# Kernel optimization log

Hardware: AMD Instinct MI355X
Metric: run time of the kernel (lower is better)

The kernel has to match this reference:

```python
import jax, jax.numpy as jnp
import numpy as np

FP8_MAX = 448.0  # float8_e4m3fn max representable magnitude


def _to_fp8(x):
    # round-to-nearest fp8_e4m3 simulation via dtype cast
    return jnp.clip(x, -FP8_MAX, FP8_MAX).astype(jnp.float8_e4m3fn).astype(jnp.float32)


def setup_inputs() -> dict:
    key = jax.random.key(0)
    ks = jax.random.split(key, 8)
    T, H, I, E, K = 4096, 2048, 4096, 8, 2

    x = jax.random.normal(ks[0], (T, H), dtype=jnp.float32)
    selected_experts = jax.random.randint(ks[1], (T, K), 0, E, dtype=jnp.int32)
    rw = jax.random.uniform(ks[2], (T, K), dtype=jnp.float32) + 1e-3
    routing_weights = rw / jnp.sum(rw, axis=-1, keepdims=True)

    # float master weights -> per-tensor fp8 quantized buffers + weight scales
    w1_f = jax.random.normal(ks[3], (E, 2 * I, H), dtype=jnp.float32) * 0.02
    w2_f = jax.random.normal(ks[4], (E, H, I), dtype=jnp.float32) * 0.02
    w1_wscale = jnp.max(jnp.abs(w1_f), axis=(1, 2)) / FP8_MAX  # [E]
    w2_wscale = jnp.max(jnp.abs(w2_f), axis=(1, 2)) / FP8_MAX
    w1 = _to_fp8(w1_f / w1_wscale[:, None, None])  # fp8 values stored as f32
    w2 = _to_fp8(w2_f / w2_wscale[:, None, None])

    # per-tensor activation input scales (amax-style calibration constants)
    w1_iscale = jnp.full((E,), 4.0 / FP8_MAX, dtype=jnp.float32)
    w2_iscale = jnp.full((E,), 8.0 / FP8_MAX, dtype=jnp.float32)

    return {
        "x": x,
        "selected_experts": selected_experts,
        "routing_weights": routing_weights,
        "w1": w1,
        "w2": w2,
        "w1_iscale": w1_iscale,
        "w2_iscale": w2_iscale,
        "w1_wscale": w1_wscale,
        "w2_wscale": w2_wscale,
    }


def _fp8_linear(x, w_fp8, iscale, wscale):
    xq = _to_fp8(x / iscale)  # [T, in]
    return (xq @ w_fp8.T) * (iscale * wscale)  # [T, out]


def reference(x, selected_experts, routing_weights, w1, w2,
              w1_iscale, w2_iscale, w1_wscale, w2_wscale):
    E = w1.shape[0]
    I = w2.shape[2]
    out = jnp.zeros_like(x)
    for e in range(E):  # fixed small expert loop
        # combined routing weight for this expert per token: [T]
        gate = jnp.sum(
            jnp.where(selected_experts == e, routing_weights, 0.0), axis=-1)
        h = _fp8_linear(x, w1[e], w1_iscale[e], w1_wscale[e])  # [T, 2I]
        g, u = h[:, :I], h[:, I:]
        a = jax.nn.silu(g) * u  # gated activation
        y = _fp8_linear(a, w2[e], w2_iscale[e], w2_wscale[e])  # [T, H]
        out = out + gate[:, None] * y
    return out
```

## Files before the change

kernel.cpp:

```cpp
#include <hip/hip_runtime.h>
#include <cstdint>
#include <cstddef>

#define T_TOK 4096
#define H_DIM 2048
#define I_DIM 4096
#define E_NUM 8
#define CAP_ROWS 9216

#define OFF_COUNTS   0
#define OFF_CURSOR   64
#define OFF_PADOFF   128
#define OFF_TOKIDX   1024
#define OFF_TOKGATE  (OFF_TOKIDX + CAP_ROWS*4)
#define OFF_XQ       ((size_t)(OFF_TOKGATE + CAP_ROWS*4))
#define XQ_BYTES     ((size_t)CAP_ROWS*H_DIM*2)
#define OFF_AQ       (OFF_XQ + XQ_BYTES)
#define AQ_BYTES     ((size_t)CAP_ROWS*I_DIM*2)
#define OFF_W1B      (OFF_AQ + AQ_BYTES)
#define W1B_BYTES    ((size_t)E_NUM*2*I_DIM*H_DIM*2)
#define OFF_W2B      (OFF_W1B + W1B_BYTES)

typedef __bf16 bf16x8 __attribute__((ext_vector_type(8)));
typedef float  f32x4  __attribute__((ext_vector_type(4)));

__device__ __forceinline__ unsigned short bf16hi(float f) {
  return (unsigned short)(__float_as_uint(f) >> 16);
}

__device__ __forceinline__ float fp8_round(float v) {
  v = fminf(448.f, fmaxf(-448.f, v));
  float av = fabsf(v);
  if (av < 0.015625f) {
    return rintf(v * 512.f) * (1.f / 512.f);
  }
  unsigned u = __float_as_uint(v);
  unsigned lsb = (u >> 20) & 1u;
  u += 0x7FFFFu + lsb;
  u &= 0xFFF00000u;
  return __uint_as_float(u);
}

__device__ __forceinline__ void gld16(const void* g, void* l) {
  __builtin_amdgcn_global_load_lds(
      (__attribute__((address_space(1))) void*)((void*)g),
      (__attribute__((address_space(3))) void*)l, 16, 0, 0);
}

__global__ void k_count(const int* __restrict__ se, int* __restrict__ counts) {
  int t = blockIdx.x * 256 + threadIdx.x;
  if (t >= T_TOK) return;
  int e0 = se[t * 2], e1 = se[t * 2 + 1];
  atomicAdd(&counts[e0], 1);
  if (e1 != e0) atomicAdd(&counts[e1], 1);
}

__global__ void k_offsets(const int* __restrict__ counts, int* __restrict__ padOff) {
  if (threadIdx.x == 0 && blockIdx.x == 0) {
    int acc = 0;
    for (int e = 0; e < E_NUM; e++) {
      padOff[e] = acc;
      acc += ((counts[e] + 127) / 128) * 128;
    }
    padOff[E_NUM] = acc;
  }
}

__global__ void k_fill(const int* __restrict__ se, const float* __restrict__ rw,
                       const int* __restrict__ padOff, int* __restrict__ cursor,
                       int* __restrict__ tokIdx, float* __restrict__ tokGate) {
  int t = blockIdx.x * 256 + threadIdx.x;
  if (t >= T_TOK) return;
  int e0 = se[t * 2], e1 = se[t * 2 + 1];
  float w0 = rw[t * 2], w1 = rw[t * 2 + 1];
  float g0 = w0 + (e1 == e0 ? w1 : 0.f);
  int s0 = atomicAdd(&cursor[e0], 1);
  tokIdx[padOff[e0] + s0] = t;
  tokGate[padOff[e0] + s0] = g0;
  if (e1 != e0) {
    int s1 = atomicAdd(&cursor[e1], 1);
    tokIdx[padOff[e1] + s1] = t;
    tokGate[padOff[e1] + s1] = w1;
  }
}

__global__ __launch_bounds__(256)
void k_gather(const float* __restrict__ x, const int* __restrict__ padOff,
              const int* __restrict__ counts, const int* __restrict__ tokIdx,
              const float* __restrict__ w1_is, unsigned short* __restrict__ xq) {
  const int rblk = blockIdx.x;
  const int total = padOff[E_NUM];
  if (rblk >= total) return;
  int e = 0;
  while (rblk >= padOff[e + 1]) e++;
  unsigned short* dst = xq + (size_t)rblk * H_DIM;
  const int c = threadIdx.x * 8;
  const int local = rblk - padOff[e];
  if (local >= counts[e]) {
    uint4 z = {0u, 0u, 0u, 0u};
    *(uint4*)(dst + c) = z;
    return;
  }
  const int tok = tokIdx[rblk];
  const float is = w1_is[e];
  const float* src = x + (size_t)tok * H_DIM + c;
  float4 v0 = *(const float4*)(src);
  float4 v1 = *(const float4*)(src + 4);
  float q0 = fp8_round(v0.x / is), q1 = fp8_round(v0.y / is);
  float q2 = fp8_round(v0.z / is), q3 = fp8_round(v0.w / is);
  float q4 = fp8_round(v1.x / is), q5 = fp8_round(v1.y / is);
  float q6 = fp8_round(v1.z / is), q7 = fp8_round(v1.w / is);
  uint4 o;
  o.x = (unsigned)bf16hi(q0) | ((unsigned)bf16hi(q1) << 16);
  o.y = (unsigned)bf16hi(q2) | ((unsigned)bf16hi(q3) << 16);
  o.z = (unsigned)bf16hi(q4) | ((unsigned)bf16hi(q5) << 16);
  o.w = (unsigned)bf16hi(q6) | ((unsigned)bf16hi(q7) << 16);
  *(uint4*)(dst + c) = o;
}

__global__ __launch_bounds__(256)
void k_wconv(const float* __restrict__ w, unsigned short* __restrict__ o, long n4) {
  long i = (long)blockIdx.x * 256 + threadIdx.x;
  if (i >= n4) return;
  float4 v = ((const float4*)w)[i];
  ushort4 r;
  r.x = bf16hi(v.x); r.y = bf16hi(v.y); r.z = bf16hi(v.z); r.w = bf16hi(v.w);
  ((ushort4*)o)[i] = r;
}

__global__ __launch_bounds__(512, 1)
void k_gemm1(const unsigned short* __restrict__ xq,
             const unsigned short* __restrict__ w1b,
             const int* __restrict__ padOff,
             const float* __restrict__ w1_is, const float* __restrict__ w1_ws,
             const float* __restrict__ w2_is,
             unsigned short* __restrict__ aq) {
  const int e = blockIdx.z;
  const int rbase = padOff[e];
  const int rows = padOff[e + 1] - rbase;
  const int mt = blockIdx.y;
  if (mt * 128 >= rows) return;
  const int nt = blockIdx.x;

  __shared__ __align__(16) unsigned short As[128 * 32];
  __shared__ __align__(16) unsigned short Bg[128 * 32];
  __shared__ __align__(16) unsigned short Bu[128 * 32];

  const int tid = threadIdx.x;
  const int lane = tid & 63;
  const int wave = tid >> 6;
  const int wm = wave >> 2, wn = wave & 3;
  const int lr = lane & 15, quad = lane >> 4;

  const int r = tid >> 2;
  const int kb = tid & 3;
  const unsigned short* pa = xq + (size_t)(rbase + mt * 128 + r) * H_DIM + kb * 8;
  const unsigned short* pg = w1b + ((size_t)e * 2 * I_DIM + nt * 128 + r) * H_DIM + kb * 8;
  const unsigned short* pu = pg + (size_t)I_DIM * H_DIM;
  unsigned short* la = As + tid * 8;
  unsigned short* lg = Bg + tid * 8;
  unsigned short* lu = Bu + tid * 8;

  f32x4 accg[4][2] = {};
  f32x4 accu[4][2] = {};

  for (int k0 = 0; k0 < H_DIM; k0 += 32) {
    gld16(pa + k0, la);
    gld16(pg + k0, lg);
    gld16(pu + k0, lu);
    __syncthreads();
    bf16x8 af[4], gf[2], uf[2];
#pragma unroll
    for (int i = 0; i < 4; i++)
      af[i] = *(const bf16x8*)(As + (wm * 64 + i * 16 + lr) * 32 + quad * 8);
#pragma unroll
    for (int j = 0; j < 2; j++) {
      gf[j] = *(const bf16x8*)(Bg + (wn * 32 + j * 16 + lr) * 32 + quad * 8);
      uf[j] = *(const bf16x8*)(Bu + (wn * 32 + j * 16 + lr) * 32 + quad * 8);
    }
#pragma unroll
    for (int i = 0; i < 4; i++)
#pragma unroll
      for (int j = 0; j < 2; j++) {
        accg[i][j] = __builtin_amdgcn_mfma_f32_16x16x32_bf16(af[i], gf[j], accg[i][j], 0, 0, 0);
        accu[i][j] = __builtin_amdgcn_mfma_f32_16x16x32_bf16(af[i], uf[j], accu[i][j], 0, 0, 0);
      }
    __syncthreads();
  }

  const float s1 = w1_is[e] * w1_ws[e];
  const float is2 = w2_is[e];
#pragma unroll
  for (int i = 0; i < 4; i++)
#pragma unroll
    for (int j = 0; j < 2; j++)
#pragma unroll
      for (int rr = 0; rr < 4; rr++) {
        const int row = wm * 64 + i * 16 + quad * 4 + rr;
        const int col = nt * 128 + wn * 32 + j * 16 + lr;
        float g = accg[i][j][rr] * s1;
        float u = accu[i][j][rr] * s1;
        float a = (g / (1.f + expf(-g))) * u;
        float q = fp8_round(a / is2);
        aq[(size_t)(rbase + mt * 128 + row) * I_DIM + col] = bf16hi(q);
      }
}

__global__ __launch_bounds__(512, 1)
void k_gemm2(const unsigned short* __restrict__ aq,
             const unsigned short* __restrict__ w2b,
             const int* __restrict__ padOff, const int* __restrict__ counts,
             const int* __restrict__ tokIdx, const float* __restrict__ tokGate,
             const float* __restrict__ w2_is, const float* __restrict__ w2_ws,
             float* __restrict__ out) {
  const int e = blockIdx.z;
  const int rbase = padOff[e];
  const int rows = padOff[e + 1] - rbase;
  const int mt = blockIdx.y;
  if (mt * 128 >= rows) return;
  const int nt = blockIdx.x;
  const int cnt = counts[e];

  __shared__ __align__(16) unsigned short As[128 * 32];
  __shared__ __align__(16) unsigned short Bs[128 * 32];
  __shared__ int sTok[128];
  __shared__ float sGate[128];

  const int tid = threadIdx.x;
  const int lane = tid & 63;
  const int wave = tid >> 6;
  const int wm = wave >> 2, wn = wave & 3;
  const int lr = lane & 15, quad = lane >> 4;

  if (tid < 128) {
    int rr = mt * 128 + tid;
    if (rr < cnt) { sTok[tid] = tokIdx[rbase + rr]; sGate[tid] = tokGate[rbase + rr]; }
    else          { sTok[tid] = -1;                 sGate[tid] = 0.f; }
  }

  const int r = tid >> 2;
  const int kb = tid & 3;
  const unsigned short* pa = aq + (size_t)(rbase + mt * 128 + r) * I_DIM + kb * 8;
  const unsigned short* pb = w2b + ((size_t)e * H_DIM + nt * 128 + r) * I_DIM + kb * 8;
  unsigned short* la = As + tid * 8;
  unsigned short* lb = Bs + tid * 8;

  f32x4 acc[4][2] = {};

  for (int k0 = 0; k0 < I_DIM; k0 += 32) {
    gld16(pa + k0, la);
    gld16(pb + k0, lb);
    __syncthreads();
    bf16x8 af[4], bf[2];
#pragma unroll
    for (int i = 0; i < 4; i++)
      af[i] = *(const bf16x8*)(As + (wm * 64 + i * 16 + lr) * 32 + quad * 8);
#pragma unroll
    for (int j = 0; j < 2; j++)
      bf[j] = *(const bf16x8*)(Bs + (wn * 32 + j * 16 + lr) * 32 + quad * 8);
#pragma unroll
    for (int i = 0; i < 4; i++)
#pragma unroll
      for (int j = 0; j < 2; j++)
        acc[i][j] = __builtin_amdgcn_mfma_f32_16x16x32_bf16(af[i], bf[j], acc[i][j], 0, 0, 0);
    __syncthreads();
  }

  const float s2 = w2_is[e] * w2_ws[e];
#pragma unroll
  for (int i = 0; i < 4; i++)
#pragma unroll
    for (int j = 0; j < 2; j++)
#pragma unroll
      for (int rr = 0; rr < 4; rr++) {
        const int row = wm * 64 + i * 16 + quad * 4 + rr;
        const int tk = sTok[row];
        if (tk >= 0) {
          const int col = nt * 128 + wn * 32 + j * 16 + lr;
          unsafeAtomicAdd(out + (size_t)tk * H_DIM + col, sGate[row] * s2 * acc[i][j][rr]);
        }
      }
}

extern "C" void kernel_launch(void* const* d_in, const int* in_sizes, int n_in,
                              void* d_out, int out_size, void* d_ws, size_t ws_size,
                              hipStream_t stream) {
  const float* x     = (const float*)d_in[0];
  const int*   se    = (const int*)d_in[1];
  const float* rw    = (const float*)d_in[2];
  const float* w1    = (const float*)d_in[3];
  const float* w2    = (const float*)d_in[4];
  const float* w1_is = (const float*)d_in[5];
  const float* w2_is = (const float*)d_in[6];
  const float* w1_ws = (const float*)d_in[7];
  const float* w2_ws = (const float*)d_in[8];
  float* out = (float*)d_out;
  char* ws = (char*)d_ws;

  int*   counts  = (int*)(ws + OFF_COUNTS);
  int*   cursor  = (int*)(ws + OFF_CURSOR);
  int*   padOff  = (int*)(ws + OFF_PADOFF);
  int*   tokIdx  = (int*)(ws + OFF_TOKIDX);
  float* tokGate = (float*)(ws + OFF_TOKGATE);
  unsigned short* xq  = (unsigned short*)(ws + OFF_XQ);
  unsigned short* aq  = (unsigned short*)(ws + OFF_AQ);
  unsigned short* w1b = (unsigned short*)(ws + OFF_W1B);
  unsigned short* w2b = (unsigned short*)(ws + OFF_W2B);

  hipMemsetAsync(ws, 0, 1024, stream);
  hipMemsetAsync(d_out, 0, (size_t)T_TOK * H_DIM * sizeof(float), stream);

  k_count  <<<16, 256, 0, stream>>>(se, counts);
  k_offsets<<<1, 1, 0, stream>>>(counts, padOff);
  k_fill   <<<16, 256, 0, stream>>>(se, rw, padOff, cursor, tokIdx, tokGate);
  k_gather <<<CAP_ROWS, 256, 0, stream>>>(x, padOff, counts, tokIdx, w1_is, xq);

  k_wconv<<<131072, 256, 0, stream>>>(w1, w1b, (long)E_NUM * 2 * I_DIM * H_DIM / 4);
  k_wconv<<< 65536, 256, 0, stream>>>(w2, w2b, (long)E_NUM * H_DIM * I_DIM / 4);

  dim3 g1(I_DIM / 128, 32, E_NUM);
  k_gemm1<<<g1, 512, 0, stream>>>(xq, w1b, padOff, w1_is, w1_ws, w2_is, aq);

  dim3 g2(H_DIM / 128, 32, E_NUM);
  k_gemm2<<<g2, 512, 0, stream>>>(aq, w2b, padOff, counts, tokIdx, tokGate, w2_is, w2_ws, out);
}
```

Measured before the change: 1.590 ms.

## Switch expert GEMMs from bf16 to native fp8 MFMA with swizzled LDS

Stores quantized activations and weights as packed e4m3 bytes instead of bf16, and runs both expert GEMMs with the fp8 MFMA instruction over a 64-wide K tile. This halves the bytes moved for weights and activations, including the weight conversion writes, and uses the higher-throughput fp8 matrix path. It also adds an XOR swizzle on the LDS layout to reduce bank conflicts. Correctness now depends on the hand-written fp8 encoder matching e4m3fn for subnormals and on the byte-ordering assumptions of the fp8 MFMA operands.

```diff
diff --git a/kernel.cpp b/kernel.cpp
--- a/kernel.cpp
+++ b/kernel.cpp
@@ -14,19 +14,14 @@
 #define OFF_TOKIDX   1024
 #define OFF_TOKGATE  (OFF_TOKIDX + CAP_ROWS*4)
 #define OFF_XQ       ((size_t)(OFF_TOKGATE + CAP_ROWS*4))
-#define XQ_BYTES     ((size_t)CAP_ROWS*H_DIM*2)
+#define XQ_BYTES     ((size_t)CAP_ROWS*H_DIM)
 #define OFF_AQ       (OFF_XQ + XQ_BYTES)
-#define AQ_BYTES     ((size_t)CAP_ROWS*I_DIM*2)
+#define AQ_BYTES     ((size_t)CAP_ROWS*I_DIM)
 #define OFF_W1B      (OFF_AQ + AQ_BYTES)
-#define W1B_BYTES    ((size_t)E_NUM*2*I_DIM*H_DIM*2)
+#define W1B_BYTES    ((size_t)E_NUM*2*I_DIM*H_DIM)
 #define OFF_W2B      (OFF_W1B + W1B_BYTES)
 
-typedef __bf16 bf16x8 __attribute__((ext_vector_type(8)));
-typedef float  f32x4  __attribute__((ext_vector_type(4)));
-
-__device__ __forceinline__ unsigned short bf16hi(float f) {
-  return (unsigned short)(__float_as_uint(f) >> 16);
-}
+typedef float f32x4 __attribute__((ext_vector_type(4)));
 
 __device__ __forceinline__ float fp8_round(float v) {
   v = fminf(448.f, fmaxf(-448.f, v));
@@ -39,6 +34,18 @@
   u += 0x7FFFFu + lsb;
   u &= 0xFFF00000u;
   return __uint_as_float(u);
+}
+
+__device__ __forceinline__ unsigned fp8_enc(float q) {
+  unsigned u = __float_as_uint(q);
+  unsigned s = (u >> 24) & 0x80u;
+  float aq = fabsf(q);
+  if (aq < 0.015625f) {
+    return s | (unsigned)(int)rintf(aq * 512.f);
+  }
+  unsigned e = (u >> 23) & 0xFFu;
+  unsigned man = (u >> 20) & 7u;
+  return s | ((e - 120u) << 3) | man;
 }
 
 __device__ __forceinline__ void gld16(const void* g, void* l) {
@@ -87,18 +94,17 @@
 __global__ __launch_bounds__(256)
 void k_gather(const float* __restrict__ x, const int* __restrict__ padOff,
               const int* __restrict__ counts, const int* __restrict__ tokIdx,
-              const float* __restrict__ w1_is, unsigned short* __restrict__ xq) {
+              const float* __restrict__ w1_is, unsigned char* __restrict__ xq) {
   const int rblk = blockIdx.x;
   const int total = padOff[E_NUM];
   if (rblk >= total) return;
   int e = 0;
   while (rblk >= padOff[e + 1]) e++;
-  unsigned short* dst = xq + (size_t)rblk * H_DIM;
+  unsigned char* dst = xq + (size_t)rblk * H_DIM;
   const int c = threadIdx.x * 8;
   const int local = rblk - padOff[e];
   if (local >= counts[e]) {
-    uint4 z = {0u, 0u, 0u, 0u};
-    *(uint4*)(dst + c) = z;
+    *(uint2*)(dst + c) = make_uint2(0u, 0u);
     return;
   }
   const int tok = tokIdx[rblk];
@@ -106,35 +112,36 @@
   const float* src = x + (size_t)tok * H_DIM + c;
   float4 v0 = *(const float4*)(src);
   float4 v1 = *(const float4*)(src + 4);
-  float q0 = fp8_round(v0.x / is), q1 = fp8_round(v0.y / is);
-  float q2 = fp8_round(v0.z / is), q3 = fp8_round(v0.w / is);
-  float q4 = fp8_round(v1.x / is), q5 = fp8_round(v1.y / is);
-  float q6 = fp8_round(v1.z / is), q7 = fp8_round(v1.w / is);
-  uint4 o;
-  o.x = (unsigned)bf16hi(q0) | ((unsigned)bf16hi(q1) << 16);
-  o.y = (unsigned)bf16hi(q2) | ((unsigned)bf16hi(q3) << 16);
-  o.z = (unsigned)bf16hi(q4) | ((unsigned)bf16hi(q5) << 16);
-  o.w = (unsigned)bf16hi(q6) | ((unsigned)bf16hi(q7) << 16);
-  *(uint4*)(dst + c) = o;
+  unsigned lo = fp8_enc(fp8_round(v0.x / is))
+              | (fp8_enc(fp8_round(v0.y / is)) << 8)
+              | (fp8_enc(fp8_round(v0.z / is)) << 16)
+              | (fp8_enc(fp8_round(v0.w / is)) << 24);
+  unsigned hi = fp8_enc(fp8_round(v1.x / is))
+              | (fp8_enc(fp8_round(v1.y / is)) << 8)
+              | (fp8_enc(fp8_round(v1.z / is)) << 16)
+              | (fp8_enc(fp8_round(v1.w / is)) << 24);
+  *(uint2*)(dst + c) = make_uint2(lo, hi);
 }
 
 __global__ __launch_bounds__(256)
-void k_wconv(const float* __restrict__ w, unsigned short* __restrict__ o, long n4) {
+void k_wconv(const float* __restrict__ w, unsigned char* __restrict__ o, long n8) {
   long i = (long)blockIdx.x * 256 + threadIdx.x;
-  if (i >= n4) return;
-  float4 v = ((const float4*)w)[i];
-  ushort4 r;
-  r.x = bf16hi(v.x); r.y = bf16hi(v.y); r.z = bf16hi(v.z); r.w = bf16hi(v.w);
-  ((ushort4*)o)[i] = r;
+  if (i >= n8) return;
+  const float4* src = (const float4*)w + i * 2;
+  float4 v0 = src[0];
+  float4 v1 = src[1];
+  unsigned lo = fp8_enc(v0.x) | (fp8_enc(v0.y) << 8) | (fp8_enc(v0.z) << 16) | (fp8_enc(v0.w) << 24);
+  unsigned hi = fp8_enc(v1.x) | (fp8_enc(v1.y) << 8) | (fp8_enc(v1.z) << 16) | (fp8_enc(v1.w) << 24);
+  ((uint2*)o)[i] = make_uint2(lo, hi);
 }
 
 __global__ __launch_bounds__(512, 1)
-void k_gemm1(const unsigned short* __restrict__ xq,
-             const unsigned short* __restrict__ w1b,
+void k_gemm1(const unsigned char* __restrict__ xq,
+             const unsigned char* __restrict__ w1b,
              const int* __restrict__ padOff,
              const float* __restrict__ w1_is, const float* __restrict__ w1_ws,
              const float* __restrict__ w2_is,
-             unsigned short* __restrict__ aq) {
+             unsigned char* __restrict__ aq) {
   const int e = blockIdx.z;
   const int rbase = padOff[e];
   const int rows = padOff[e + 1] - rbase;
@@ -142,48 +149,62 @@
   if (mt * 128 >= rows) return;
   const int nt = blockIdx.x;
 
-  __shared__ __align__(16) unsigned short As[128 * 32];
-  __shared__ __align__(16) unsigned short Bg[128 * 32];
-  __shared__ __align__(16) unsigned short Bu[128 * 32];
+  __shared__ __align__(16) unsigned char As[128 * 64];
+  __shared__ __align__(16) unsigned char Bg[128 * 64];
+  __shared__ __align__(16) unsigned char Bu[128 * 64];
 
   const int tid = threadIdx.x;
   const int lane = tid & 63;
   const int wave = tid >> 6;
   const int wm = wave >> 2, wn = wave & 3;
   const int lr = lane & 15, quad = lane >> 4;
+  const int qh = quad >> 1, ql = quad & 1;
+  const int swz = (lr >> 2) & 3;
+  const int cs0 = (((0 + qh) ^ swz) << 4) + ql * 8;
+  const int cs1 = (((2 + qh) ^ swz) << 4) + ql * 8;
 
   const int r = tid >> 2;
   const int kb = tid & 3;
-  const unsigned short* pa = xq + (size_t)(rbase + mt * 128 + r) * H_DIM + kb * 8;
-  const unsigned short* pg = w1b + ((size_t)e * 2 * I_DIM + nt * 128 + r) * H_DIM + kb * 8;
-  const unsigned short* pu = pg + (size_t)I_DIM * H_DIM;
-  unsigned short* la = As + tid * 8;
-  unsigned short* lg = Bg + tid * 8;
-  unsigned short* lu = Bu + tid * 8;
+  const int kbs = (kb ^ ((r >> 2) & 3)) * 16;
+  const unsigned char* pa = xq + (size_t)(rbase + mt * 128 + r) * H_DIM + kbs;
+  const unsigned char* pg = w1b + ((size_t)e * 2 * I_DIM + nt * 128 + r) * H_DIM + kbs;
+  const unsigned char* pu = pg + (size_t)I_DIM * H_DIM;
+  unsigned char* la = As + tid * 16;
+  unsigned char* lg = Bg + tid * 16;
+  unsigned char* lu = Bu + tid * 16;
 
   f32x4 accg[4][2] = {};
   f32x4 accu[4][2] = {};
 
-  for (int k0 = 0; k0 < H_DIM; k0 += 32) {
+  for (int k0 = 0; k0 < H_DIM; k0 += 64) {
     gld16(pa + k0, la);
     gld16(pg + k0, lg);
     gld16(pu + k0, lu);
     __syncthreads();
-    bf16x8 af[4], gf[2], uf[2];
+    long af[4][2], gf[2][2], uf[2][2];
+#pragma unroll
+    for (int i = 0; i < 4; i++) {
+      const unsigned char* ba = As + (wm * 64 + i * 16 + lr) * 64;
+      af[i][0] = *(const long*)(ba + cs0);
+      af[i][1] = *(const long*)(ba + cs1);
+    }
+#pragma unroll
+    for (int j = 0; j < 2; j++) {
+      const unsigned char* bg = Bg + (wn * 32 + j * 16 + lr) * 64;
+      const unsigned char* bu = Bu + (wn * 32 + j * 16 + lr) * 64;
+      gf[j][0] = *(const long*)(bg + cs0);
+      gf[j][1] = *(const long*)(bg + cs1);
+      uf[j][0] = *(const long*)(bu + cs0);
+      uf[j][1] = *(const long*)(bu + cs1);
+    }
 #pragma unroll
     for (int i = 0; i < 4; i++)
-      af[i] = *(const bf16x8*)(As + (wm * 64 + i * 16 + lr) * 32 + quad * 8);
-#pragma unroll
-    for (int j = 0; j < 2; j++) {
-      gf[j] = *(const bf16x8*)(Bg + (wn * 32 + j * 16 + lr) * 32 + quad * 8);
-      uf[j] = *(const bf16x8*)(Bu + (wn * 32 + j * 16 + lr) * 32 + quad * 8);
-    }
-#pragma unroll
-    for (int i = 0; i < 4; i++)
 #pragma unroll
       for (int j = 0; j < 2; j++) {
-        accg[i][j] = __builtin_amdgcn_mfma_f32_16x16x32_bf16(af[i], gf[j], accg[i][j], 0, 0, 0);
-        accu[i][j] = __builtin_amdgcn_mfma_f32_16x16x32_bf16(af[i], uf[j], accu[i][j], 0, 0, 0);
+        accg[i][j] = __builtin_amdgcn_mfma_f32_16x16x32_fp8_fp8(af[i][0], gf[j][0], accg[i][j], 0, 0, 0);
+        accg[i][j] = __builtin_amdgcn_mfma_f32_16x16x32_fp8_fp8(af[i][1], gf[j][1], accg[i][j], 0, 0, 0);
+        accu[i][j] = __builtin_amdgcn_mfma_f32_16x16x32_fp8_fp8(af[i][0], uf[j][0], accu[i][j], 0, 0, 0);
+        accu[i][j] = __builtin_amdgcn_mfma_f32_16x16x32_fp8_fp8(af[i][1], uf[j][1], accu[i][j], 0, 0, 0);
       }
     __syncthreads();
   }
@@ -202,13 +223,13 @@
         float u = accu[i][j][rr] * s1;
         float a = (g / (1.f + expf(-g))) * u;
         float q = fp8_round(a / is2);
-        aq[(size_t)(rbase + mt * 128 + row) * I_DIM + col] = bf16hi(q);
+        aq[(size_t)(rbase + mt * 128 + row) * I_DIM + col] = (unsigned char)fp8_enc(q);
       }
 }
 
 __global__ __launch_bounds__(512, 1)
-void k_gemm2(const unsigned short* __restrict__ aq,
-             const unsigned short* __restrict__ w2b,
+void k_gemm2(const unsigned char* __restrict__ aq,
+             const unsigned char* __restrict__ w2b,
              const int* __restrict__ padOff, const int* __restrict__ counts,
              const int* __restrict__ tokIdx, const float* __restrict__ tokGate,
              const float* __restrict__ w2_is, const float* __restrict__ w2_ws,
@@ -221,8 +242,8 @@
   const int nt = blockIdx.x;
   const int cnt = counts[e];
 
-  __shared__ __align__(16) unsigned short As[128 * 32];
-  __shared__ __align__(16) unsigned short Bs[128 * 32];
+  __shared__ __align__(16) unsigned char As[128 * 64];
+  __shared__ __align__(16) unsigned char Bs[128 * 64];
   __shared__ int sTok[128];
   __shared__ float sGate[128];
 
@@ -231,6 +252,10 @@
   const int wave = tid >> 6;
   const int wm = wave >> 2, wn = wave & 3;
   const int lr = lane & 15, quad = lane >> 4;
+  const int qh = quad >> 1, ql = quad & 1;
+  const int swz = (lr >> 2) & 3;
+  const int cs0 = (((0 + qh) ^ swz) << 4) + ql * 8;
+  const int cs1 = (((2 + qh) ^ swz) << 4) + ql * 8;
 
   if (tid < 128) {
     int rr = mt * 128 + tid;
@@ -240,29 +265,38 @@
 
   const int r = tid >> 2;
   const int kb = tid & 3;
-  const unsigned short* pa = aq + (size_t)(rbase + mt * 128 + r) * I_DIM + kb * 8;
-  const unsigned short* pb = w2b + ((size_t)e * H_DIM + nt * 128 + r) * I_DIM + kb * 8;
-  unsigned short* la = As + tid * 8;
-  unsigned short* lb = Bs + tid * 8;
+  const int kbs = (kb ^ ((r >> 2) & 3)) * 16;
+  const unsigned char* pa = aq + (size_t)(rbase + mt * 128 + r) * I_DIM + kbs;
+  const unsigned char* pb = w2b + ((size_t)e * H_DIM + nt * 128 + r) * I_DIM + kbs;
+  unsigned char* la = As + tid * 16;
+  unsigned char* lb = Bs + tid * 16;
 
   f32x4 acc[4][2] = {};
 
-  for (int k0 = 0; k0 < I_DIM; k0 += 32) {
+  for (int k0 = 0; k0 < I_DIM; k0 += 64) {
     gld16(pa + k0, la);
     gld16(pb + k0, lb);
     __syncthreads();
-    bf16x8 af[4], bf[2];
+    long af[4][2], bf[2][2];
+#pragma unroll
+    for (int i = 0; i < 4; i++) {
+      const unsigned char* ba = As + (wm * 64 + i * 16 + lr) * 64;
+      af[i][0] = *(const long*)(ba + cs0);
+      af[i][1] = *(const long*)(ba + cs1);
+    }
+#pragma unroll
+    for (int j = 0; j < 2; j++) {
+      const unsigned char* bb = Bs + (wn * 32 + j * 16 + lr) * 64;
+      bf[j][0] = *(const long*)(bb + cs0);
+      bf[j][1] = *(const long*)(bb + cs1);
+    }
 #pragma unroll
     for (int i = 0; i < 4; i++)
-      af[i] = *(const bf16x8*)(As + (wm * 64 + i * 16 + lr) * 32 + quad * 8);
-#pragma unroll
-    for (int j = 0; j < 2; j++)
-      bf[j] = *(const bf16x8*)(Bs + (wn * 32 + j * 16 + lr) * 32 + quad * 8);
-#pragma unroll
-    for (int i = 0; i < 4; i++)
-#pragma unroll
-      for (int j = 0; j < 2; j++)
-        acc[i][j] = __builtin_amdgcn_mfma_f32_16x16x32_bf16(af[i], bf[j], acc[i][j], 0, 0, 0);
+#pragma unroll
+      for (int j = 0; j < 2; j++) {
+        acc[i][j] = __builtin_amdgcn_mfma_f32_16x16x32_fp8_fp8(af[i][0], bf[j][0], acc[i][j], 0, 0, 0);
+        acc[i][j] = __builtin_amdgcn_mfma_f32_16x16x32_fp8_fp8(af[i][1], bf[j][1], acc[i][j], 0, 0, 0);
+      }
     __syncthreads();
   }
 
@@ -302,10 +336,10 @@
   int*   padOff  = (int*)(ws + OFF_PADOFF);
   int*   tokIdx  = (int*)(ws + OFF_TOKIDX);
   float* tokGate = (float*)(ws + OFF_TOKGATE);
-  unsigned short* xq  = (unsigned short*)(ws + OFF_XQ);
-  unsigned short* aq  = (unsigned short*)(ws + OFF_AQ);
-  unsigned short* w1b = (unsigned short*)(ws + OFF_W1B);
-  unsigned short* w2b = (unsigned short*)(ws + OFF_W2B);
+  unsigned char* xq  = (unsigned char*)(ws + OFF_XQ);
+  unsigned char* aq  = (unsigned char*)(ws + OFF_AQ);
+  unsigned char* w1b = (unsigned char*)(ws + OFF_W1B);
+  unsigned char* w2b = (unsigned char*)(ws + OFF_W2B);
 
   hipMemsetAsync(ws, 0, 1024, stream);
   hipMemsetAsync(d_out, 0, (size_t)T_TOK * H_DIM * sizeof(float), stream);
@@ -315,8 +349,8 @@
   k_fill   <<<16, 256, 0, stream>>>(se, rw, padOff, cursor, tokIdx, tokGate);
   k_gather <<<CAP_ROWS, 256, 0, stream>>>(x, padOff, counts, tokIdx, w1_is, xq);
 
-  k_wconv<<<131072, 256, 0, stream>>>(w1, w1b, (long)E_NUM * 2 * I_DIM * H_DIM / 4);
-  k_wconv<<< 65536, 256, 0, stream>>>(w2, w2b, (long)E_NUM * H_DIM * I_DIM / 4);
+  k_wconv<<<65536, 256, 0, stream>>>(w1, w1b, (long)E_NUM * 2 * I_DIM * H_DIM / 8);
+  k_wconv<<<32768, 256, 0, stream>>>(w2, w2b, (long)E_NUM * H_DIM * I_DIM / 8);
 
   dim3 g1(I_DIM / 128, 32, E_NUM);
   k_gemm1<<<g1, 512, 0, stream>>>(xq, w1b, padOff, w1_is, w1_ws, w2_is, aq);
```

Measured after the change: 1.386 ms. 12.8% less time.
